# Kernel tuning notes

Measured on AMD Instinct MI355X. Metric: run time of the kernel, lower is better.

The kernel has to match this reference:

```python
import jax, jax.numpy as jnp
import numpy as np

N = 100000   # nodes
E = 1600000  # edges
F = 64       # node_features == latent_channels
H = 128      # hidden_channels
G = 256      # graphs
L = 2        # n_layers


def setup_inputs() -> dict:
    key = jax.random.key(0)
    ks = jax.random.split(key, 20)
    x = jax.random.normal(ks[0], (N, F), dtype=jnp.float32)
    u = jax.random.normal(ks[1], (G, 2), dtype=jnp.float32)
    edge_index = jax.random.randint(ks[2], (2, E), 0, N, dtype=jnp.int32)
    # evenly assign nodes to graphs (sorted segment ids, no empty segments)
    batch = (jnp.arange(N, dtype=jnp.int32) * G // N).astype(jnp.int32)
    s = 0.05
    # per-layer edge-MLP params, stacked over layers: in = 2F-2 = 126
    W1 = jax.random.normal(ks[3], (L, 2 * F - 2, H), dtype=jnp.float32) * s
    b1 = jnp.zeros((L, H), dtype=jnp.float32)
    W2 = jax.random.normal(ks[4], (L, H, H), dtype=jnp.float32) * s
    b2 = jnp.zeros((L, H), dtype=jnp.float32)
    W3 = jax.random.normal(ks[5], (L, H, F), dtype=jnp.float32) * s
    b3 = jnp.zeros((L, F), dtype=jnp.float32)
    # readout head: in = 3*F + 2 = 194
    LW1 = jax.random.normal(ks[6], (3 * F + 2, F), dtype=jnp.float32) * s
    Lb1 = jnp.zeros((F,), dtype=jnp.float32)
    LW2 = jax.random.normal(ks[7], (F, F), dtype=jnp.float32) * s
    Lb2 = jnp.zeros((F,), dtype=jnp.float32)
    LW3 = jax.random.normal(ks[8], (F, 2), dtype=jnp.float32) * s
    Lb3 = jnp.zeros((2,), dtype=jnp.float32)
    return dict(x=x, u=u, edge_index=edge_index, batch=batch,
                W1=W1, b1=b1, W2=W2, b2=b2, W3=W3, b3=b3,
                LW1=LW1, Lb1=Lb1, LW2=LW2, Lb2=Lb2, LW3=LW3, Lb3=Lb3)


def _edge_layer(x, src, dst, W1, b1, W2, b2, W3, b3):
    xi = x[dst]            # target nodes (x_i), [E, F]
    xj = x[src]            # source nodes (x_j), [E, F]
    d = xj[:, :3] - xi[:, :3]
    dist2 = jnp.sum(d * d, axis=-1, keepdims=True)  # [E, 1]
    m_in = jnp.concatenate([xi, xj[:, 3:], dist2], axis=-1)  # [E, 2F-2]
    h = jax.nn.silu(m_in @ W1 + b1)
    h = jax.nn.silu(h @ W2 + b2)
    m = jax.nn.silu(h @ W3 + b3)                    # [E, F]
    return jax.ops.segment_sum(m, dst, num_segments=N)  # aggr='sum'


def reference(x, u, edge_index, batch, W1, b1, W2, b2, W3, b3,
              LW1, Lb1, LW2, Lb2, LW3, Lb3):
    src, dst = edge_index[0], edge_index[1]
    for l in range(L):
        x = _edge_layer(x, src, dst, W1[l], b1[l], W2[l], b2[l], W3[l], b3[l])
    addp = jax.ops.segment_sum(x, batch, num_segments=G)
    cnt = jax.ops.segment_sum(jnp.ones((N, 1), x.dtype), batch, num_segments=G)
    meanp = addp / jnp.maximum(cnt, 1.0)
    maxp = jax.ops.segment_max(x, batch, num_segments=G)
    pooled = jnp.concatenate([addp, meanp, maxp, u], axis=1)  # [G, 3F+2]
    h = jax.nn.silu(pooled @ LW1 + Lb1)
    h = jax.nn.silu(h @ LW2 + Lb2)
    return h @ LW3 + Lb3  # [G, 2]
```

## Files before the change

kernel.cpp:

```cpp
#include <hip/hip_runtime.h>
#include <hip/hip_bf16.h>

typedef _Float16 f16;
typedef _Float16 f16x8 __attribute__((ext_vector_type(8)));
typedef float    f32x4 __attribute__((ext_vector_type(4)));
typedef float    f32x8 __attribute__((ext_vector_type(8)));

__device__ __forceinline__ float silu_f(float x) {
    return x * __builtin_amdgcn_rcpf(1.0f + __expf(-x));
}

__device__ __forceinline__ void load_lds16(const f16* g, f16* l) {
    __builtin_amdgcn_global_load_lds(
        (const __attribute__((address_space(1))) void*)g,
        (__attribute__((address_space(3))) void*)l, 16, 0, 0);
}

__global__ void prep_kernel(const float* __restrict__ W1, const float* __restrict__ W2,
                            const float* __restrict__ W3, f16* __restrict__ B1T,
                            f16* __restrict__ W2T, f16* __restrict__ W3T,
                            f16* __restrict__ w1c, int L, int total) {
    int idx = blockIdx.x * 256 + threadIdx.x;
    if (idx >= total) return;
    const int per = 16384 + 16384 + 8192 + 128;
    int l = idx / per, r = idx % per;
    const float* W1l = W1 + (size_t)l * 126 * 128;
    if (r < 16384) {
        int c = r >> 6, k = r & 63;
        float v;
        if (c < 128) v = W1l[k * 128 + c];
        else v = (k >= 3) ? W1l[(64 + k - 3) * 128 + (c - 128)]
                          : 0.0f;
        B1T[(size_t)l * 16384 + r] = (f16)v;
    } else if (r < 32768) {
        int q = r - 16384, n = q >> 7, k = q & 127;
        W2T[(size_t)l * 16384 + q] = (f16)W2[(size_t)l * 16384 + k * 128 + n];
    } else if (r < 40960) {
        int q = r - 32768, n = q >> 7, k = q & 127;
        W3T[(size_t)l * 8192 + q] = (f16)W3[(size_t)l * 8192 + k * 64 + n];
    } else {
        int c = r - 40960;
        w1c[l * 128 + c] = (f16)W1l[125 * 128 + c];
    }
}

__global__ void hist_kernel(const int* __restrict__ ei, int* __restrict__ deg, int E) {
    int i = blockIdx.x * 256 + threadIdx.x;
    if (i < E) atomicAdd(&deg[ei[E + i]], 1);
}

__global__ void scan_part(const int* __restrict__ deg, int* __restrict__ bsum, int N) {
    __shared__ int red[256];
    int t = threadIdx.x;
    int i = blockIdx.x * 256 + t;
    red[t] = (i < N) ? deg[i] : 0;
    __syncthreads();
    for (int s = 128; s > 0; s >>= 1) {
        if (t < s) red[t] += red[t + s];
        __syncthreads();
    }
    if (t == 0) bsum[blockIdx.x] = red[0];
}

__global__ void scan_mid(const int* __restrict__ bsum, int* __restrict__ boff, int nb) {
    __shared__ int sm[512];
    int t = threadIdx.x;
    int v = (t < nb) ? bsum[t] : 0;
    sm[t] = v;
    __syncthreads();
    for (int off = 1; off < 512; off <<= 1) {
        int a = (t >= off) ? sm[t - off] : 0;
        __syncthreads();
        sm[t] += a;
        __syncthreads();
    }
    if (t < nb) boff[t] = sm[t] - v;
}

__global__ void scan_final(const int* __restrict__ deg, const int* __restrict__ boff,
                           int* __restrict__ row_start, int N) {
    __shared__ int sm[256];
    int t = threadIdx.x;
    int i = blockIdx.x * 256 + t;
    int v = (i < N) ? deg[i] : 0;
    sm[t] = v;
    __syncthreads();
    for (int off = 1; off < 256; off <<= 1) {
        int a = (t >= off) ? sm[t - off] : 0;
        __syncthreads();
        sm[t] += a;
        __syncthreads();
    }
    if (i < N) row_start[i] = boff[blockIdx.x] + sm[t] - v;
}

__global__ void scatter_kernel(const int* __restrict__ ei, const int* __restrict__ row_start,
                               int* __restrict__ cursor, int* __restrict__ srcs,
                               int* __restrict__ dsts, int E) {
    int i = blockIdx.x * 256 + threadIdx.x;
    if (i < E) {
        int d = ei[E + i];
        int p = row_start[d] + atomicAdd(&cursor[d], 1);
        srcs[p] = ei[i];
        dsts[p] = d;
    }
}

__global__ __launch_bounds__(256, 3) void node_kernel(
    const float* __restrict__ x, const f16* __restrict__ B1T,
    const float* __restrict__ b1, f16* __restrict__ PQ,
    float4* __restrict__ C, int N, int ntiles) {
    __shared__ f16 b1t[256 * 72];
    const int tid = threadIdx.x;
    const int w = tid >> 6, lane = tid & 63, lm = lane & 15, kg = lane >> 4;

    for (int i = tid; i < 256 * 64; i += 256)
        b1t[(i >> 6) * 72 + (i & 63)] = B1T[i];
    __syncthreads();

    for (int tile = blockIdx.x; tile < ntiles; tile += gridDim.x) {
        const int base = tile * 64;
        int ar = base + w * 16 + lm;
        if (ar >= N) ar = N - 1;

        f16x8 afrag[2];
#pragma unroll
        for (int ks = 0; ks < 2; ks++) {
            f32x8 v = *(const f32x8*)(x + (size_t)ar * 64 + ks * 32 + kg * 8);
            f16x8 h;
#pragma unroll
            for (int j = 0; j < 8; j++) h[j] = (f16)v[j];
            afrag[ks] = h;
        }

        f32x4 acc[16];
#pragma unroll
        for (int nb = 0; nb < 16; nb++) acc[nb] = (f32x4){0.f, 0.f, 0.f, 0.f};
#pragma unroll
        for (int ks = 0; ks < 2; ks++)
#pragma unroll
            for (int nb = 0; nb < 16; nb++) {
                f16x8 b = *(const f16x8*)&b1t[(nb * 16 + lm) * 72 + ks * 32 + kg * 8];
                acc[nb] = __builtin_amdgcn_mfma_f32_16x16x32_f16(afrag[ks], b, acc[nb], 0, 0, 0);
            }

#pragma unroll
        for (int nb = 0; nb < 16; nb++) {
            int col = nb * 16 + lm;
            float bias = (col < 128) ? b1[col] : 0.0f;
#pragma unroll
            for (int reg = 0; reg < 4; reg++) {
                int orow = base + w * 16 + kg * 4 + reg;
                if (orow < N) PQ[(size_t)orow * 256 + col] = (f16)(acc[nb][reg] + bias);
            }
        }
        if (tid < 64) {
            int n = base + tid;
            if (n < N) {
                const float* xr = x + (size_t)n * 64;
                C[n] = make_float4(xr[0], xr[1], xr[2], 0.0f);
            }
        }
    }
}

__global__ __launch_bounds__(256, 2) void edge_kernel(
    const f16* __restrict__ PQ, const float4* __restrict__ C,
    const int* __restrict__ srcs, const int* __restrict__ dsts,
    const f16* __restrict__ W2T, const f16* __restrict__ W3T,
    const f16* __restrict__ w1c, const float* __restrict__ b2,
    const float* __restrict__ b3, float* __restrict__ xout,
    int E, int wtiles) {
    __shared__ f16 w2t[128 * 128];
    __shared__ f16 stage[4 * 4096];
    __shared__ f16 tb[2 * 4 * 576];

    const int tid = threadIdx.x;
    const int w = tid >> 6, lane = tid & 63, lm = lane & 15, kg = lane >> 4;
    const int e4 = lane >> 2, c4 = lane & 3;

    for (int i = tid; i < 128 * 128; i += 256) {
        int n = i >> 7, k = i & 127;
        w2t[n * 128 + (((k >> 3) ^ (n & 15)) << 3) + (k & 7)] = W2T[i];
    }

    f16x8 wvh[4];
#pragma unroll
    for (int ks = 0; ks < 4; ks++) wvh[ks] = *(const f16x8*)(w1c + ks * 32 + kg * 8);
    float bias2[8], bias3[4];
#pragma unroll
    for (int nb = 0; nb < 8; nb++) bias2[nb] = b2[nb * 16 + lm];
#pragma unroll
    for (int nb = 0; nb < 4; nb++) bias3[nb] = b3[nb * 16 + lm];
    __syncthreads();

    f16* sw = stage + w * 4096;
    const int nwaves = gridDim.x * 4;

    int t = blockIdx.x * 4 + w;
    int e0 = t * 16 + lm;
    int erc = min(e0, E - 1);
    int scl = srcs[erc];
    int dcl = dsts[erc];
    int dsen = (e0 < E) ? dcl : -1;
    float4 cs = C[scl], cd = C[dcl];
    {
        int de = __shfl(dcl, e4), se = __shfl(scl, e4);
        const f16* gp = PQ + (size_t)de * 256 + c4 * 8;
        const f16* gq = PQ + (size_t)se * 256 + 128 + c4 * 8;
#pragma unroll
        for (int j = 0; j < 4; j++) load_lds16(gp + j * 32, sw + j * 512 + lane * 8);
#pragma unroll
        for (int j = 0; j < 4; j++) load_lds16(gq + j * 32, sw + 2048 + j * 512 + lane * 8);
    }

    while (t < wtiles) {
        const int tn = t + nwaves;

        int e1 = tn * 16 + lm;
        int erc2 = min(e1, E - 1);
        int s2c = srcs[erc2];
        int d2c = dsts[erc2];
        asm volatile("s_waitcnt vmcnt(2)" ::: "memory");

        float dx = cs.x - cd.x, dy = cs.y - cd.y, dz = cs.z - cd.z;
        float dist2 = dx * dx + dy * dy + dz * dz;

        f16x8 afrag[4];
#pragma unroll
        for (int ks = 0; ks < 4; ks++) {
            f16x8 p = *(const f16x8*)&sw[ks * 512 + lm * 32 + kg * 8];
            f16x8 q = *(const f16x8*)&sw[2048 + ks * 512 + lm * 32 + kg * 8];
            f16x8 h;
#pragma unroll
            for (int j = 0; j < 8; j++) {
                float v = (float)p[j] + (float)q[j] + dist2 * (float)wvh[ks][j];
                h[j] = (f16)silu_f(v);
            }
            afrag[ks] = h;
        }

        f32x4 acc1[8];
#pragma unroll
        for (int nb = 0; nb < 8; nb++) acc1[nb] = (f32x4){0.f, 0.f, 0.f, 0.f};
#pragma unroll
        for (int ks = 0; ks < 4; ks++)
#pragma unroll
            for (int nb = 0; nb < 8; nb++) {
                int n = nb * 16 + lm;
                f16x8 b = *(const f16x8*)&w2t[n * 128 + (((ks * 4 + kg) ^ (n & 15)) << 3)];
                acc1[nb] = __builtin_amdgcn_mfma_f32_16x16x32_f16(afrag[ks], b, acc1[nb], 0, 0, 0);
            }

        const int d2sen = (e1 < E) ? d2c : -1;
        const float4 cs2 = C[s2c], cd2 = C[d2c];
        asm volatile("" ::: "memory");
        if (tn < wtiles) {
            int de = __shfl(d2c, e4), se = __shfl(s2c, e4);
            const f16* gp = PQ + (size_t)de * 256 + c4 * 8;
            const f16* gq = PQ + (size_t)se * 256 + 128 + c4 * 8;
#pragma unroll
            for (int j = 0; j < 4; j++) load_lds16(gp + j * 32, sw + j * 512 + lane * 8);
#pragma unroll
            for (int j = 0; j < 4; j++) load_lds16(gq + j * 32, sw + 2048 + j * 512 + lane * 8);
        }

        f32x4 acc2[4];
#pragma unroll
        for (int nb2 = 0; nb2 < 4; nb2++) acc2[nb2] = (f32x4){0.f, 0.f, 0.f, 0.f};
#pragma unroll
        for (int kq = 0; kq < 4; kq++) {
            f16* tq = tb + (kq & 1) * (4 * 576) + w * 576;
#pragma unroll
            for (int nn = 0; nn < 2; nn++) {
                int nb = kq * 2 + nn;
#pragma unroll
                for (int reg = 0; reg < 4; reg++)
                    tq[(kg * 4 + reg) * 36 + nn * 16 + lm] =
                        (f16)silu_f(acc1[nb][reg] + bias2[nb]);
            }
            f16x8 a2 = *(const f16x8*)&tq[lm * 36 + kg * 8];
#pragma unroll
            for (int nb2 = 0; nb2 < 4; nb2++) {
                f16x8 b = *(const f16x8*)(W3T + (size_t)(nb2 * 16 + lm) * 128 +
                                          kq * 32 + kg * 8);
                acc2[nb2] = __builtin_amdgcn_mfma_f32_16x16x32_f16(a2, b, acc2[nb2], 0, 0, 0);
            }
        }

        {
            const int r0 = kg * 4;
            const int dr0 = __shfl(dsen, r0);
            const int dr1 = __shfl(dsen, r0 + 1);
            const int dr2 = __shfl(dsen, r0 + 2);
            const int dr3 = __shfl(dsen, r0 + 3);
            int prevv = __shfl(dsen, (r0 - 1) & 63);
            if (kg == 0) prevv = -1234567;

            const bool e01 = dr0 == dr1, e12 = dr1 == dr2, e23 = dr2 == dr3;
            const bool c01 = e01, c02 = e01 && e12, c03 = c02 && e23;
            const bool c12 = e12, c13 = e12 && e23;
            const int fullI = c03 ? 1 : 0;

            const int tgt = dr3;
            const int l1i = (lane + 16) & 63, l2i = (lane + 32) & 63, l3i = (lane + 48) & 63;
            const int dr0_1 = __shfl(dr0, l1i), fu1 = __shfl(fullI, l1i);
            const int dr0_2 = __shfl(dr0, l2i), fu2 = __shfl(fullI, l2i);
            const int dr0_3 = __shfl(dr0, l3i);
            const bool take1 = (kg <= 2) && (dr0_1 == tgt);
            const bool take2 = take1 && fu1 && (kg <= 1) && (dr0_2 == tgt);
            const bool take3 = take2 && fu2 && (kg == 0) && (dr0_3 == tgt);

            const bool h0 = (dr0 != prevv) && (dr0 >= 0);
            const bool h1f = (!e01) && (dr1 >= 0);
            const bool h2f = (!e12) && (dr2 >= 0);
            const bool h3f = (!e23) && (dr3 >= 0);

            float t0v[4], t1v[4], t2v[4], t3v[4];
#pragma unroll
            for (int nb2 = 0; nb2 < 4; nb2++) {
                const float bias = bias3[nb2];
                const float v0 = silu_f(acc2[nb2][0] + bias);
                const float v1 = silu_f(acc2[nb2][1] + bias);
                const float v2 = silu_f(acc2[nb2][2] + bias);
                const float v3 = silu_f(acc2[nb2][3] + bias);
                float lead = v0 + (c01 ? v1 : 0.f) + (c02 ? v2 : 0.f) + (c03 ? v3 : 0.f);
                float ext = 0.f;
                const float le1 = __shfl(lead, l1i);
                const float le2 = __shfl(lead, l2i);
                const float le3 = __shfl(lead, l3i);
                if (take1) ext += le1;
                if (take2) ext += le2;
                if (take3) ext += le3;
                t0v[nb2] = lead + (c03 ? ext : 0.f);
                t1v[nb2] = v1 + (c12 ? v2 : 0.f) + (c13 ? (v3 + ext) : 0.f);
                t2v[nb2] = v2 + (e23 ? (v3 + ext) : 0.f);
                t3v[nb2] = v3 + ext;
            }
            if (h0) {
                float* p = xout + (size_t)dr0 * 64 + lm;
#pragma unroll
                for (int nb2 = 0; nb2 < 4; nb2++) atomicAdd(p + nb2 * 16, t0v[nb2]);
            }
            if (h1f) {
                float* p = xout + (size_t)dr1 * 64 + lm;
#pragma unroll
                for (int nb2 = 0; nb2 < 4; nb2++) atomicAdd(p + nb2 * 16, t1v[nb2]);
            }
            if (h2f) {
                float* p = xout + (size_t)dr2 * 64 + lm;
#pragma unroll
                for (int nb2 = 0; nb2 < 4; nb2++) atomicAdd(p + nb2 * 16, t2v[nb2]);
            }
            if (h3f) {
                float* p = xout + (size_t)dr3 * 64 + lm;
#pragma unroll
                for (int nb2 = 0; nb2 < 4; nb2++) atomicAdd(p + nb2 * 16, t3v[nb2]);
            }
        }

        t = tn;
        scl = s2c; dcl = d2c; dsen = d2sen;
        cs = cs2; cd = cd2;
    }
    asm volatile("s_waitcnt vmcnt(0)" ::: "memory");
}

__global__ void pool_kernel(const float* __restrict__ xf, const float* __restrict__ u,
                            float* __restrict__ pooled, int N, int G) {
    int g = blockIdx.x;
    int t = threadIdx.x;
    int ch = t & 63, sub = t >> 6;
    long long n0 = ((long long)g * N + G - 1) / G;
    long long n1 = ((long long)(g + 1) * N + G - 1) / G;
    float sm = 0.f, mx = -3.0e38f;
    for (long long n = n0 + sub; n < n1; n += 4) {
        float v = xf[n * 64 + ch];
        sm += v;
        mx = fmaxf(mx, v);
    }
    __shared__ float ssum[256], smax[256];
    ssum[t] = sm;
    smax[t] = mx;
    __syncthreads();
    if (sub == 0) {
        float a = ssum[ch] + ssum[64 + ch] + ssum[128 + ch] + ssum[192 + ch];
        float m = fmaxf(fmaxf(smax[ch], smax[64 + ch]), fmaxf(smax[128 + ch], smax[192 + ch]));
        float cnt = (float)(n1 - n0);
        pooled[g * 194 + ch] = a;
        pooled[g * 194 + 64 + ch] = a / fmaxf(cnt, 1.f);
        pooled[g * 194 + 128 + ch] = m;
    }
    if (t == 0) {
        pooled[g * 194 + 192] = u[g * 2];
        pooled[g * 194 + 193] = u[g * 2 + 1];
    }
}

__global__ void head_kernel(const float* __restrict__ pooled,
                            const float* __restrict__ LW1, const float* __restrict__ Lb1,
                            const float* __restrict__ LW2, const float* __restrict__ Lb2,
                            const float* __restrict__ LW3, const float* __restrict__ Lb3,
                            float* __restrict__ out, int G) {
    int g = blockIdx.x, t = threadIdx.x;
    __shared__ float pl[194];
    __shared__ float hl[64];
    for (int k = t; k < 194; k += 64) pl[k] = pooled[g * 194 + k];
    __syncthreads();
    float a = Lb1[t];
    for (int k = 0; k < 194; k++) a += pl[k] * LW1[k * 64 + t];
    a = a / (1.0f + __expf(-a));
    hl[t] = a;
    __syncthreads();
    float b = Lb2[t];
    for (int k = 0; k < 64; k++) b += hl[k] * LW2[k * 64 + t];
    b = b / (1.0f + __expf(-b));
    __syncthreads();
    hl[t] = b;
    __syncthreads();
    if (t < 2) {
        float c = Lb3[t];
        for (int k = 0; k < 64; k++) c += hl[k] * LW3[k * 2 + t];
        out[g * 2 + t] = c;
    }
}

extern "C" void kernel_launch(void* const* d_in, const int* in_sizes, int n_in,
                              void* d_out, int out_size, void* d_ws, size_t ws_size,
                              hipStream_t stream) {
    const float* x   = (const float*)d_in[0];
    const float* u   = (const float*)d_in[1];
    const int*   ei  = (const int*)d_in[2];
    const float* W1  = (const float*)d_in[4];
    const float* b1  = (const float*)d_in[5];
    const float* W2  = (const float*)d_in[6];
    const float* b2  = (const float*)d_in[7];
    const float* W3  = (const float*)d_in[8];
    const float* b3  = (const float*)d_in[9];
    const float* LW1 = (const float*)d_in[10];
    const float* Lb1 = (const float*)d_in[11];
    const float* LW2 = (const float*)d_in[12];
    const float* Lb2 = (const float*)d_in[13];
    const float* LW3 = (const float*)d_in[14];
    const float* Lb3 = (const float*)d_in[15];

    const int N = in_sizes[0] / 64;
    const int G = in_sizes[1] / 2;
    const int E = in_sizes[2] / 2;
    const int L = in_sizes[4] / (126 * 128);

    char* ws = (char*)d_ws;
    size_t off = 0;
    auto alloc = [&](size_t bytes) -> char* {
        char* p = ws + off;
        off += (bytes + 511) & ~(size_t)511;
        return p;
    };
    f16*    PQ     = (f16*)alloc((size_t)N * 256 * 2);
    float4* C      = (float4*)alloc((size_t)N * 16);
    float*  x1     = (float*)alloc((size_t)N * 64 * 4);
    float*  x2     = (float*)alloc((size_t)N * 64 * 4);
    int*    srcs   = (int*)alloc((size_t)E * 4);
    int*    dsts   = (int*)alloc((size_t)E * 4);
    int*    deg    = (int*)alloc((size_t)N * 4);
    int*    rowst  = (int*)alloc((size_t)N * 4);
    int*    cursor = (int*)alloc((size_t)N * 4);
    int*    bsum   = (int*)alloc(4096);
    int*    boff   = (int*)alloc(4096);
    f16*    B1T    = (f16*)alloc((size_t)L * 256 * 64 * 2);
    f16*    W2T    = (f16*)alloc((size_t)L * 128 * 128 * 2);
    f16*    W3T    = (f16*)alloc((size_t)L * 64 * 128 * 2);
    f16*    w1c    = (f16*)alloc((size_t)L * 128 * 2);
    float*  pooled = (float*)alloc((size_t)G * 194 * 4);
    (void)ws_size;
    (void)n_in;
    (void)out_size;

    hipMemsetAsync(deg, 0, (size_t)N * 4, stream);
    hipMemsetAsync(cursor, 0, (size_t)N * 4, stream);
    hipMemsetAsync(x1, 0, (size_t)N * 64 * 4, stream);
    hipMemsetAsync(x2, 0, (size_t)N * 64 * 4, stream);

    {
        int total = L * (16384 + 16384 + 8192 + 128);
        prep_kernel<<<(total + 255) / 256, 256, 0, stream>>>(W1, W2, W3, B1T, W2T, W3T, w1c, L, total);
    }
    hist_kernel<<<(E + 255) / 256, 256, 0, stream>>>(ei, deg, E);
    int NB = (N + 255) / 256;
    scan_part<<<NB, 256, 0, stream>>>(deg, bsum, N);
    scan_mid<<<1, 512, 0, stream>>>(bsum, boff, NB);
    scan_final<<<NB, 256, 0, stream>>>(deg, boff, rowst, N);
    scatter_kernel<<<(E + 255) / 256, 256, 0, stream>>>(ei, rowst, cursor, srcs, dsts, E);

    const float* xcur = x;
    const int wtiles = (E + 15) / 16;
    const int ntiles_node = (N + 63) / 64;
    for (int l = 0; l < L; l++) {
        node_kernel<<<768, 256, 0, stream>>>(xcur, B1T + (size_t)l * 16384, b1 + l * 128,
                                             PQ, C, N, ntiles_node);
        float* xo = (l & 1) ? x2 : x1;
        edge_kernel<<<512, 256, 0, stream>>>(PQ, C, srcs, dsts,
                                             W2T + (size_t)l * 16384, W3T + (size_t)l * 8192,
                                             w1c + l * 128, b2 + l * 128, b3 + l * 64,
                                             xo, E, wtiles);
        xcur = xo;
    }
    pool_kernel<<<G, 256, 0, stream>>>(xcur, u, pooled, N, G);
    head_kernel<<<G, 64, 0, stream>>>(pooled, LW1, Lb1, LW2, Lb2, LW3, Lb3, (float*)d_out, G);
}
```

Measured before the change: 1.024 ms.

## Software-pipeline edge kernel: defer epilogue atomics one tile, prefetch indices two tiles ahead

Restructures the edge-kernel loop so each tile's silu/segmented-reduction/atomicAdd epilogue runs one iteration later, overlapping it with the next tile's first MFMA stage. Edge indices are now prefetched two tiles ahead and node coords one ahead, and the PQ gather is issued before the second GEMM rather than after the first. It also widens the per-wave transpose buffer so two K-slices are written before reading, and does the p+q add in packed fp16 with fp32 W1 weights. This raises register pressure (extra acc2p and prefetch registers) and adds a duplicated tail epilogue, and the fp16 p+q add slightly changes rounding.

```diff
diff --git a/kernel.cpp b/kernel.cpp
--- a/kernel.cpp
+++ b/kernel.cpp
@@ -173,7 +173,7 @@
     int E, int wtiles) {
     __shared__ f16 w2t[128 * 128];
     __shared__ f16 stage[4 * 4096];
-    __shared__ f16 tb[2 * 4 * 576];
+    __shared__ f16 tb[4 * 16 * 72];
 
     const int tid = threadIdx.x;
     const int w = tid >> 6, lane = tid & 63, lm = lane & 15, kg = lane >> 4;
@@ -184,9 +184,13 @@
         w2t[n * 128 + (((k >> 3) ^ (n & 15)) << 3) + (k & 7)] = W2T[i];
     }
 
-    f16x8 wvh[4];
-#pragma unroll
-    for (int ks = 0; ks < 4; ks++) wvh[ks] = *(const f16x8*)(w1c + ks * 32 + kg * 8);
+    f32x8 wvh[4];
+#pragma unroll
+    for (int ks = 0; ks < 4; ks++) {
+        f16x8 wv = *(const f16x8*)(w1c + ks * 32 + kg * 8);
+#pragma unroll
+        for (int j = 0; j < 8; j++) wvh[ks][j] = (float)wv[j];
+    }
     float bias2[8], bias3[4];
 #pragma unroll
     for (int nb = 0; nb < 8; nb++) bias2[nb] = b2[nb * 16 + lm];
@@ -195,15 +199,18 @@
     __syncthreads();
 
     f16* sw = stage + w * 4096;
+    f16* tq = tb + w * (16 * 72);
     const int nwaves = gridDim.x * 4;
+    const int r0 = kg * 4;
+    const int l1i = (lane + 16) & 63, l2i = (lane + 32) & 63, l3i = (lane + 48) & 63;
 
     int t = blockIdx.x * 4 + w;
+    if (t >= wtiles) return;
     int e0 = t * 16 + lm;
     int erc = min(e0, E - 1);
     int scl = srcs[erc];
     int dcl = dsts[erc];
-    int dsen = (e0 < E) ? dcl : -1;
-    float4 cs = C[scl], cd = C[dcl];
+    int dsen_cur = (e0 < E) ? dcl : -1;
     {
         int de = __shfl(dcl, e4), se = __shfl(scl, e4);
         const f16* gp = PQ + (size_t)de * 256 + c4 * 8;
@@ -213,15 +220,22 @@
 #pragma unroll
         for (int j = 0; j < 4; j++) load_lds16(gq + j * 32, sw + 2048 + j * 512 + lane * 8);
     }
-
-    while (t < wtiles) {
+    int e1 = (t + nwaves) * 16 + lm;
+    int erc1 = min(max(e1, 0), E - 1);
+    int s_nx = srcs[erc1];
+    int d_nx = dsts[erc1];
+    int e_nx_ok = (e1 < E) ? 1 : 0;
+    float4 cs = C[scl], cd = C[dcl];
+
+    f32x4 acc2p[4];
+#pragma unroll
+    for (int nb2 = 0; nb2 < 4; nb2++) acc2p[nb2] = (f32x4){0.f, 0.f, 0.f, 0.f};
+    int dsen_prev = -1;
+
+    while (true) {
         const int tn = t + nwaves;
 
-        int e1 = tn * 16 + lm;
-        int erc2 = min(e1, E - 1);
-        int s2c = srcs[erc2];
-        int d2c = dsts[erc2];
-        asm volatile("s_waitcnt vmcnt(2)" ::: "memory");
+        asm volatile("s_waitcnt vmcnt(4)" ::: "memory");
 
         float dx = cs.x - cd.x, dy = cs.y - cd.y, dz = cs.z - cd.z;
         float dist2 = dx * dx + dy * dy + dz * dz;
@@ -231,10 +245,11 @@
         for (int ks = 0; ks < 4; ks++) {
             f16x8 p = *(const f16x8*)&sw[ks * 512 + lm * 32 + kg * 8];
             f16x8 q = *(const f16x8*)&sw[2048 + ks * 512 + lm * 32 + kg * 8];
+            f16x8 pq = p + q;
             f16x8 h;
 #pragma unroll
             for (int j = 0; j < 8; j++) {
-                float v = (float)p[j] + (float)q[j] + dist2 * (float)wvh[ks][j];
+                float v = (float)pq[j] + dist2 * wvh[ks][j];
                 h[j] = (f16)silu_f(v);
             }
             afrag[ks] = h;
@@ -252,49 +267,12 @@
                 acc1[nb] = __builtin_amdgcn_mfma_f32_16x16x32_f16(afrag[ks], b, acc1[nb], 0, 0, 0);
             }
 
-        const int d2sen = (e1 < E) ? d2c : -1;
-        const float4 cs2 = C[s2c], cd2 = C[d2c];
-        asm volatile("" ::: "memory");
-        if (tn < wtiles) {
-            int de = __shfl(d2c, e4), se = __shfl(s2c, e4);
-            const f16* gp = PQ + (size_t)de * 256 + c4 * 8;
-            const f16* gq = PQ + (size_t)se * 256 + 128 + c4 * 8;
-#pragma unroll
-            for (int j = 0; j < 4; j++) load_lds16(gp + j * 32, sw + j * 512 + lane * 8);
-#pragma unroll
-            for (int j = 0; j < 4; j++) load_lds16(gq + j * 32, sw + 2048 + j * 512 + lane * 8);
-        }
-
-        f32x4 acc2[4];
-#pragma unroll
-        for (int nb2 = 0; nb2 < 4; nb2++) acc2[nb2] = (f32x4){0.f, 0.f, 0.f, 0.f};
-#pragma unroll
-        for (int kq = 0; kq < 4; kq++) {
-            f16* tq = tb + (kq & 1) * (4 * 576) + w * 576;
-#pragma unroll
-            for (int nn = 0; nn < 2; nn++) {
-                int nb = kq * 2 + nn;
-#pragma unroll
-                for (int reg = 0; reg < 4; reg++)
-                    tq[(kg * 4 + reg) * 36 + nn * 16 + lm] =
-                        (f16)silu_f(acc1[nb][reg] + bias2[nb]);
-            }
-            f16x8 a2 = *(const f16x8*)&tq[lm * 36 + kg * 8];
-#pragma unroll
-            for (int nb2 = 0; nb2 < 4; nb2++) {
-                f16x8 b = *(const f16x8*)(W3T + (size_t)(nb2 * 16 + lm) * 128 +
-                                          kq * 32 + kg * 8);
-                acc2[nb2] = __builtin_amdgcn_mfma_f32_16x16x32_f16(a2, b, acc2[nb2], 0, 0, 0);
-            }
-        }
-
         {
-            const int r0 = kg * 4;
-            const int dr0 = __shfl(dsen, r0);
-            const int dr1 = __shfl(dsen, r0 + 1);
-            const int dr2 = __shfl(dsen, r0 + 2);
-            const int dr3 = __shfl(dsen, r0 + 3);
-            int prevv = __shfl(dsen, (r0 - 1) & 63);
+            const int dr0 = __shfl(dsen_prev, r0);
+            const int dr1 = __shfl(dsen_prev, r0 + 1);
+            const int dr2 = __shfl(dsen_prev, r0 + 2);
+            const int dr3 = __shfl(dsen_prev, r0 + 3);
+            int prevv = __shfl(dsen_prev, (r0 - 1) & 63);
             if (kg == 0) prevv = -1234567;
 
             const bool e01 = dr0 == dr1, e12 = dr1 == dr2, e23 = dr2 == dr3;
@@ -303,7 +281,6 @@
             const int fullI = c03 ? 1 : 0;
 
             const int tgt = dr3;
-            const int l1i = (lane + 16) & 63, l2i = (lane + 32) & 63, l3i = (lane + 48) & 63;
             const int dr0_1 = __shfl(dr0, l1i), fu1 = __shfl(fullI, l1i);
             const int dr0_2 = __shfl(dr0, l2i), fu2 = __shfl(fullI, l2i);
             const int dr0_3 = __shfl(dr0, l3i);
@@ -320,10 +297,10 @@
 #pragma unroll
             for (int nb2 = 0; nb2 < 4; nb2++) {
                 const float bias = bias3[nb2];
-                const float v0 = silu_f(acc2[nb2][0] + bias);
-                const float v1 = silu_f(acc2[nb2][1] + bias);
-                const float v2 = silu_f(acc2[nb2][2] + bias);
-                const float v3 = silu_f(acc2[nb2][3] + bias);
+                const float v0 = silu_f(acc2p[nb2][0] + bias);
+                const float v1 = silu_f(acc2p[nb2][1] + bias);
+                const float v2 = silu_f(acc2p[nb2][2] + bias);
+                const float v3 = silu_f(acc2p[nb2][3] + bias);
                 float lead = v0 + (c01 ? v1 : 0.f) + (c02 ? v2 : 0.f) + (c03 ? v3 : 0.f);
                 float ext = 0.f;
                 const float le1 = __shfl(lead, l1i);
@@ -359,9 +336,131 @@
             }
         }
 
+        int dsen_nx = e_nx_ok ? d_nx : -1;
+        if (tn < wtiles) {
+            int de = __shfl(d_nx, e4), se = __shfl(s_nx, e4);
+            const f16* gp = PQ + (size_t)de * 256 + c4 * 8;
+            const f16* gq = PQ + (size_t)se * 256 + 128 + c4 * 8;
+#pragma unroll
+            for (int j = 0; j < 4; j++) load_lds16(gp + j * 32, sw + j * 512 + lane * 8);
+#pragma unroll
+            for (int j = 0; j < 4; j++) load_lds16(gq + j * 32, sw + 2048 + j * 512 + lane * 8);
+        }
+
+        int e2 = (tn + nwaves) * 16 + lm;
+        int erc2 = min(max(e2, 0), E - 1);
+        int s_nx2 = srcs[erc2];
+        int d_nx2 = dsts[erc2];
+        int e_nx2_ok = (e2 < E) ? 1 : 0;
+        float4 cs2 = C[s_nx], cd2 = C[d_nx];
+
+        f32x4 acc2[4];
+#pragma unroll
+        for (int nb2 = 0; nb2 < 4; nb2++) acc2[nb2] = (f32x4){0.f, 0.f, 0.f, 0.f};
+#pragma unroll
+        for (int half = 0; half < 2; half++) {
+#pragma unroll
+            for (int kqi = 0; kqi < 2; kqi++) {
+                int kq = half * 2 + kqi;
+#pragma unroll
+                for (int nn = 0; nn < 2; nn++) {
+                    int nb = kq * 2 + nn;
+#pragma unroll
+                    for (int reg = 0; reg < 4; reg++)
+                        tq[(kg * 4 + reg) * 72 + kqi * 32 + nn * 16 + lm] =
+                            (f16)silu_f(acc1[nb][reg] + bias2[nb]);
+                }
+            }
+#pragma unroll
+            for (int kqi = 0; kqi < 2; kqi++) {
+                int kq = half * 2 + kqi;
+                f16x8 a2 = *(const f16x8*)&tq[lm * 72 + kqi * 32 + kg * 8];
+#pragma unroll
+                for (int nb2 = 0; nb2 < 4; nb2++) {
+                    f16x8 b = *(const f16x8*)(W3T + (size_t)(nb2 * 16 + lm) * 128 +
+                                              kq * 32 + kg * 8);
+                    acc2[nb2] = __builtin_amdgcn_mfma_f32_16x16x32_f16(a2, b, acc2[nb2], 0, 0, 0);
+                }
+            }
+        }
+
+#pragma unroll
+        for (int nb2 = 0; nb2 < 4; nb2++) acc2p[nb2] = acc2[nb2];
+        dsen_prev = dsen_cur;
+        dsen_cur = dsen_nx;
+        s_nx = s_nx2; d_nx = d_nx2; e_nx_ok = e_nx2_ok;
+        cs = cs2; cd = cd2;
         t = tn;
-        scl = s2c; dcl = d2c; dsen = d2sen;
-        cs = cs2; cd = cd2;
+        if (t >= wtiles) break;
+    }
+
+    {
+        const int dr0 = __shfl(dsen_prev, r0);
+        const int dr1 = __shfl(dsen_prev, r0 + 1);
+        const int dr2 = __shfl(dsen_prev, r0 + 2);
+        const int dr3 = __shfl(dsen_prev, r0 + 3);
+        int prevv = __shfl(dsen_prev, (r0 - 1) & 63);
+        if (kg == 0) prevv = -1234567;
+
+        const bool e01 = dr0 == dr1, e12 = dr1 == dr2, e23 = dr2 == dr3;
+        const bool c01 = e01, c02 = e01 && e12, c03 = c02 && e23;
+        const bool c12 = e12, c13 = e12 && e23;
+        const int fullI = c03 ? 1 : 0;
+
+        const int tgt = dr3;
+        const int dr0_1 = __shfl(dr0, l1i), fu1 = __shfl(fullI, l1i);
+        const int dr0_2 = __shfl(dr0, l2i), fu2 = __shfl(fullI, l2i);
+        const int dr0_3 = __shfl(dr0, l3i);
+        const bool take1 = (kg <= 2) && (dr0_1 == tgt);
+        const bool take2 = take1 && fu1 && (kg <= 1) && (dr0_2 == tgt);
+        const bool take3 = take2 && fu2 && (kg == 0) && (dr0_3 == tgt);
+
+        const bool h0 = (dr0 != prevv) && (dr0 >= 0);
+        const bool h1f = (!e01) && (dr1 >= 0);
+        const bool h2f = (!e12) && (dr2 >= 0);
+        const bool h3f = (!e23) && (dr3 >= 0);
+
+        float t0v[4], t1v[4], t2v[4], t3v[4];
+#pragma unroll
+        for (int nb2 = 0; nb2 < 4; nb2++) {
+            const float bias = bias3[nb2];
+            const float v0 = silu_f(acc2p[nb2][0] + bias);
+            const float v1 = silu_f(acc2p[nb2][1] + bias);
+            const float v2 = silu_f(acc2p[nb2][2] + bias);
+            const float v3 = silu_f(acc2p[nb2][3] + bias);
+            float lead = v0 + (c01 ? v1 : 0.f) + (c02 ? v2 : 0.f) + (c03 ? v3 : 0.f);
+            float ext = 0.f;
+            const float le1 = __shfl(lead, l1i);
+            const float le2 = __shfl(lead, l2i);
+            const float le3 = __shfl(lead, l3i);
+            if (take1) ext += le1;
+            if (take2) ext += le2;
+            if (take3) ext += le3;
+            t0v[nb2] = lead + (c03 ? ext : 0.f);
+            t1v[nb2] = v1 + (c12 ? v2 : 0.f) + (c13 ? (v3 + ext) : 0.f);
+            t2v[nb2] = v2 + (e23 ? (v3 + ext) : 0.f);
+            t3v[nb2] = v3 + ext;
+        }
+        if (h0) {
+            float* p = xout + (size_t)dr0 * 64 + lm;
+#pragma unroll
+            for (int nb2 = 0; nb2 < 4; nb2++) atomicAdd(p + nb2 * 16, t0v[nb2]);
+        }
+        if (h1f) {
+            float* p = xout + (size_t)dr1 * 64 + lm;
+#pragma unroll
+            for (int nb2 = 0; nb2 < 4; nb2++) atomicAdd(p + nb2 * 16, t1v[nb2]);
+        }
+        if (h2f) {
+            float* p = xout + (size_t)dr2 * 64 + lm;
+#pragma unroll
+            for (int nb2 = 0; nb2 < 4; nb2++) atomicAdd(p + nb2 * 16, t2v[nb2]);
+        }
+        if (h3f) {
+            float* p = xout + (size_t)dr3 * 64 + lm;
+#pragma unroll
+            for (int nb2 = 0; nb2 < 4; nb2++) atomicAdd(p + nb2 * 16, t3v[nb2]);
+        }
     }
     asm volatile("s_waitcnt vmcnt(0)" ::: "memory");
 }
```

After: 1.035 ms. No clear change (+1.0%).
